# Kernel optimization log

Hardware: AMD Instinct MI355X
Metric: run time of the kernel (lower is better)

Reference implementation:

```python
import jax, jax.numpy as jnp
import numpy as np

N = 100000
E = 800000
D_IN = 128
D_OUT = 128
EPS = 1e-5


def setup_inputs() -> dict:
    key = jax.random.key(0)
    k = jax.random.split(key, 7)
    x = jax.random.normal(k[0], (N, D_IN), dtype=jnp.float32)
    edge_index = jax.random.randint(k[1], (2, E), 0, N, dtype=jnp.int64)
    # kaiming_uniform(a=sqrt(5)) on [out,in] -> bound = 1/sqrt(in_dim)
    bound = 1.0 / np.sqrt(D_IN)
    W_self = jax.random.uniform(k[2], (D_OUT, D_IN), minval=-bound, maxval=bound, dtype=jnp.float32)
    W_neigh = jax.random.uniform(k[3], (D_OUT, D_IN), minval=-bound, maxval=bound, dtype=jnp.float32)
    bias = jnp.zeros((D_OUT,), dtype=jnp.float32)
    gamma = jnp.ones((D_OUT,), dtype=jnp.float32)
    beta = jnp.zeros((D_OUT,), dtype=jnp.float32)
    return {"x": x, "edge_index": edge_index, "W_self": W_self,
            "W_neigh": W_neigh, "bias": bias, "gamma": gamma, "beta": beta}


def reference(x, edge_index, W_self, W_neigh, bias, gamma, beta):
    src, dst = edge_index[0], edge_index[1]
    # mean neighbor aggregation: segment-sum of gathered features / clamped degree
    agg = jax.ops.segment_sum(x[src], dst, num_segments=N)          # [N, D_IN]
    deg = jax.ops.segment_sum(jnp.ones_like(dst, dtype=x.dtype), dst, num_segments=N)
    neigh_mean = agg / jnp.maximum(deg, 1.0)[:, None]
    # dual linear + bias + ReLU
    out = jnp.einsum('nd,od->no', x, W_self) + jnp.einsum('nd,od->no', neigh_mean, W_neigh) + bias
    h = jax.nn.relu(out)
    # LayerNorm over last dim
    mu = jnp.mean(h, axis=-1, keepdims=True)
    var = jnp.var(h, axis=-1, keepdims=True)
    return (h - mu) * jax.lax.rsqrt(var + EPS) * gamma + beta
```

## Files before the change

kernel.cpp:

```cpp
#include <hip/hip_runtime.h>
#include <hip/hip_bf16.h>

#define N_NODES 100000
#define E_EDGES 800000
#define LN_EPS 1e-5f
#define WPAD 264

#define P_BLOCKS 256
#define EPB 3125
#define SLICE 64
#define NBK 1563
#define NBK_PAD 1792
#define OFFS_STRIDE 1564
#define QCAP 768
#define CONV_PER_BLOCK 12500

typedef __attribute__((ext_vector_type(4))) float f32x4;
typedef __attribute__((ext_vector_type(8))) short short8;

__device__ __forceinline__ unsigned short f2bf(float f) {
    __hip_bfloat16 h = __float2bfloat16(f);
    return *reinterpret_cast<unsigned short*>(&h);
}
__device__ __forceinline__ float bflo(unsigned int u) { return __uint_as_float(u << 16); }
__device__ __forceinline__ float bfhi(unsigned int u) { return __uint_as_float(u & 0xffff0000u); }

__global__ __launch_bounds__(256) void fill_part1(
    const float* __restrict__ x, const int* __restrict__ ei,
    unsigned short* __restrict__ xb, unsigned int* __restrict__ gstore,
    unsigned short* __restrict__ offs)
{
    const int t = threadIdx.x, b = blockIdx.x;
    if (b >= P_BLOCKS) {
        const float4* x4 = reinterpret_cast<const float4*>(x);
        ushort4* xb4 = reinterpret_cast<ushort4*>(xb);
        const int j0 = (b - P_BLOCKS) * CONV_PER_BLOCK;
        for (int j = t; j < CONV_PER_BLOCK; j += 256) {
            float4 v = x4[j0 + j];
            ushort4 o;
            o.x = f2bf(v.x); o.y = f2bf(v.y); o.z = f2bf(v.z); o.w = f2bf(v.w);
            xb4[j0 + j] = o;
        }
        return;
    }
    __shared__ unsigned long long eds[EPB];
    __shared__ unsigned int sorted_l[EPB];
    __shared__ int hist[NBK_PAD];
    __shared__ int starts[NBK_PAD + 1];
    __shared__ int partial[256];
    for (int i = t; i < NBK_PAD; i += 256) hist[i] = 0;
    __syncthreads();
    const int e0 = b * EPB;
    for (int i = t; i < EPB; i += 256) {
        unsigned src = (unsigned)ei[e0 + i];
        unsigned dst = (unsigned)ei[E_EDGES + e0 + i];
        unsigned bk = dst >> 6;
        eds[i] = ((unsigned long long)bk << 32) | (src << 6) | (dst & 63u);
        atomicAdd(&hist[bk], 1);
    }
    __syncthreads();
    int h[7], s = 0;
#pragma unroll
    for (int k = 0; k < 7; ++k) { h[k] = hist[t * 7 + k]; s += h[k]; }
    partial[t] = s;
    __syncthreads();
    for (int off = 1; off < 256; off <<= 1) {
        int v = (t >= off) ? partial[t - off] : 0;
        __syncthreads();
        partial[t] += v;
        __syncthreads();
    }
    int run = partial[t] - s;
#pragma unroll
    for (int k = 0; k < 7; ++k) { starts[t * 7 + k] = run; run += h[k]; }
    if (t == 255) starts[NBK_PAD] = run;
    __syncthreads();
    for (int i = t; i < NBK_PAD; i += 256) hist[i] = 0;
    __syncthreads();
    for (int i = t; i < EPB; i += 256) {
        unsigned long long u = eds[i];
        unsigned bk = (unsigned)(u >> 32);
        int p = starts[bk] + atomicAdd(&hist[bk], 1);
        sorted_l[p] = (unsigned int)u;
    }
    __syncthreads();
    for (int i = t; i < EPB; i += 256)
        gstore[b * EPB + i] = sorted_l[i];
    for (int i = t; i < OFFS_STRIDE; i += 256)
        offs[b * OFFS_STRIDE + i] = (unsigned short)starts[i];
}

__global__ __launch_bounds__(256) void agg2(
    const unsigned int* __restrict__ gstore, const unsigned short* __restrict__ offs,
    const unsigned short* __restrict__ xb, unsigned short* __restrict__ nb)
{
    __shared__ unsigned int sortedq[QCAP];
    __shared__ int cnt_l[SLICE];
    __shared__ int run_l[SLICE];
    __shared__ int qs_l[SLICE + 1];
    const int t = threadIdx.x, b = blockIdx.x;
    if (t < SLICE) { cnt_l[t] = 0; run_l[t] = 0; }
    __syncthreads();
    const int s0 = offs[t * OFFS_STRIDE + b];
    const int s1 = offs[t * OFFS_STRIDE + b + 1];
    const unsigned int* myrun = gstore + t * EPB;
    for (int j = s0; j < s1; ++j)
        atomicAdd(&cnt_l[myrun[j] & 63u], 1);
    __syncthreads();
    if (t < SLICE) {
        int inc = cnt_l[t];
        for (int off = 1; off < 64; off <<= 1) {
            int u = __shfl_up(inc, off);
            if (t >= off) inc += u;
        }
        qs_l[t + 1] = inc;
        if (t == 0) qs_l[0] = 0;
    }
    __syncthreads();
    for (int j = s0; j < s1; ++j) {
        unsigned rec = myrun[j];
        int p = qs_l[rec & 63u] + atomicAdd(&run_l[rec & 63u], 1);
        if (p < QCAP) sortedq[p] = rec;
    }
    __syncthreads();
    const int wave = t >> 6, lane = t & 63;
    const int subi = lane >> 4, chunk = lane & 15;
    const uint4* x4 = reinterpret_cast<const uint4*>(xb);
    for (int ln = wave * 16; ln < wave * 16 + 16; ++ln) {
        const int qb = qs_l[ln], cc = qs_l[ln + 1] - qb;
        float acc[8];
#pragma unroll
        for (int k = 0; k < 8; ++k) acc[k] = 0.f;
        for (int i = 0; i < cc; i += 4) {
            int idx = i + subi;
            if (idx < cc) {
                unsigned rec = sortedq[qb + idx];
                uint4 v = x4[(rec >> 6) * 16 + chunk];
                acc[0] += bflo(v.x); acc[1] += bfhi(v.x);
                acc[2] += bflo(v.y); acc[3] += bfhi(v.y);
                acc[4] += bflo(v.z); acc[5] += bfhi(v.z);
                acc[6] += bflo(v.w); acc[7] += bfhi(v.w);
            }
        }
#pragma unroll
        for (int k = 0; k < 8; ++k) {
            acc[k] += __shfl_xor(acc[k], 16);
            acc[k] += __shfl_xor(acc[k], 32);
        }
        const int node = b * SLICE + ln;
        if (subi == 0 && node < N_NODES) {
            float inv = 1.0f / (float)(cc > 1 ? cc : 1);
            uint4 o;
            o.x = ((unsigned)f2bf(acc[1] * inv) << 16) | f2bf(acc[0] * inv);
            o.y = ((unsigned)f2bf(acc[3] * inv) << 16) | f2bf(acc[2] * inv);
            o.z = ((unsigned)f2bf(acc[5] * inv) << 16) | f2bf(acc[4] * inv);
            o.w = ((unsigned)f2bf(acc[7] * inv) << 16) | f2bf(acc[6] * inv);
            reinterpret_cast<uint4*>(nb)[node * 16 + chunk] = o;
        }
    }
}

__global__ __launch_bounds__(256, 2) void fused_mfma(
    const unsigned short* __restrict__ xb, const unsigned short* __restrict__ nb,
    const float* __restrict__ Wself, const float* __restrict__ Wneigh,
    const float* __restrict__ bias, const float* __restrict__ gamma,
    const float* __restrict__ beta, float* __restrict__ out)
{
    __shared__ unsigned short WT[128][WPAD];
    const int t = threadIdx.x;
    const float4* Ws4 = reinterpret_cast<const float4*>(Wself);
    const float4* Wn4 = reinterpret_cast<const float4*>(Wneigh);
    for (int idx = t; idx < 4096; idx += 256) {
        int n = idx >> 5, k4 = (idx & 31) << 2;
        float4 a = Ws4[idx];
        float4 b = Wn4[idx];
        ushort4 ua, ub;
        ua.x = f2bf(a.x); ua.y = f2bf(a.y); ua.z = f2bf(a.z); ua.w = f2bf(a.w);
        ub.x = f2bf(b.x); ub.y = f2bf(b.y); ub.z = f2bf(b.z); ub.w = f2bf(b.w);
        *reinterpret_cast<ushort4*>(&WT[n][k4]) = ua;
        *reinterpret_cast<ushort4*>(&WT[n][128 + k4]) = ub;
    }
    __syncthreads();

    const int lane = t & 63, wave = t >> 6;
    const int l16 = lane & 15, quad = lane >> 4;
    float bia[8], gam[8], bet[8];
#pragma unroll
    for (int n = 0; n < 8; ++n) {
        int col = n * 16 + l16;
        bia[n] = bias[col]; gam[n] = gamma[col]; bet[n] = beta[col];
    }

    const int ntiles = (N_NODES + 255) / 256;
    for (int tile = blockIdx.x; tile < ntiles; tile += gridDim.x) {
        const int rowbase = tile * 256 + wave * 64;
        f32x4 acc[4][8];
#pragma unroll
        for (int m = 0; m < 4; ++m)
#pragma unroll
            for (int n = 0; n < 8; ++n) acc[m][n] = (f32x4)0.f;
        int rows[4];
#pragma unroll
        for (int m = 0; m < 4; ++m) {
            int r = rowbase + m * 16 + l16;
            rows[m] = r < N_NODES ? r : N_NODES - 1;
        }
#pragma unroll
        for (int kstep = 0; kstep < 8; ++kstep) {
            const unsigned short* Asrc = (kstep < 4) ? xb : nb;
            const int koff = (kstep & 3) * 32 + quad * 8;
            short8 a[4];
#pragma unroll
            for (int m = 0; m < 4; ++m)
                a[m] = *reinterpret_cast<const short8*>(Asrc + rows[m] * 128 + koff);
#pragma unroll
            for (int n = 0; n < 8; ++n) {
                short8 b = *reinterpret_cast<const short8*>(&WT[n * 16 + l16][kstep * 32 + quad * 8]);
#pragma unroll
                for (int m = 0; m < 4; ++m)
                    acc[m][n] = __builtin_amdgcn_mfma_f32_16x16x32_bf16(a[m], b, acc[m][n], 0, 0, 0);
            }
        }
#pragma unroll
        for (int m = 0; m < 4; ++m) {
#pragma unroll
            for (int r = 0; r < 4; ++r) {
                float h[8], s = 0.f, q = 0.f;
#pragma unroll
                for (int n = 0; n < 8; ++n) {
                    float v = acc[m][n][r] + bia[n];
                    v = fmaxf(v, 0.f);
                    h[n] = v; s += v; q += v * v;
                }
#pragma unroll
                for (int msk = 1; msk <= 8; msk <<= 1) {
                    s += __shfl_xor(s, msk);
                    q += __shfl_xor(q, msk);
                }
                const float mu = s * (1.f / 128.f);
                const float var = q * (1.f / 128.f) - mu * mu;
                const float rs = rsqrtf(var + LN_EPS);
                const int R = rowbase + m * 16 + quad * 4 + r;
                if (R < N_NODES) {
#pragma unroll
                    for (int n = 0; n < 8; ++n)
                        out[R * 128 + n * 16 + l16] = (h[n] - mu) * rs * gam[n] + bet[n];
                }
            }
        }
    }
}

extern "C" void kernel_launch(void* const* d_in, const int* in_sizes, int n_in,
                              void* d_out, int out_size, void* d_ws, size_t ws_size,
                              hipStream_t stream) {
    const float* x      = (const float*)d_in[0];
    const int*   ei     = (const int*)d_in[1];
    const float* Wself  = (const float*)d_in[2];
    const float* Wneigh = (const float*)d_in[3];
    const float* bias   = (const float*)d_in[4];
    const float* gamma  = (const float*)d_in[5];
    const float* beta   = (const float*)d_in[6];
    float* out = (float*)d_out;

    char* ws = (char*)d_ws;
    unsigned short* xb = (unsigned short*)ws;
    unsigned short* nb = (unsigned short*)(ws + 25600000);
    unsigned int* gstore = (unsigned int*)(ws + 51200000);
    unsigned short* offs = (unsigned short*)(ws + 54400000);

    fill_part1<<<512, 256, 0, stream>>>(x, ei, xb, gstore, offs);
    agg2<<<NBK, 256, 0, stream>>>(gstore, offs, xb, nb);
    const int ntiles = (N_NODES + 255) / 256;
    fused_mfma<<<ntiles, 256, 0, stream>>>(xb, nb, Wself, Wneigh, bias, gamma, beta, out);
}
```

Measured before the change: 204.5 us.

## Fuse neighbor aggregation with MFMA GEMM and LayerNorm in one kernel

```diff
diff --git a/kernel.cpp b/kernel.cpp
--- a/kernel.cpp
+++ b/kernel.cpp
@@ -4,7 +4,6 @@
 #define N_NODES 100000
 #define E_EDGES 800000
 #define LN_EPS 1e-5f
-#define WPAD 264
 
 #define P_BLOCKS 256
 #define EPB 3125
@@ -14,6 +13,8 @@
 #define OFFS_STRIDE 1564
 #define QCAP 768
 #define CONV_PER_BLOCK 12500
+#define TILE_BLKS 782
+#define NBPAD 136
 
 typedef __attribute__((ext_vector_type(4))) float f32x4;
 typedef __attribute__((ext_vector_type(8))) short short8;
@@ -27,8 +28,9 @@
 
 __global__ __launch_bounds__(256) void fill_part1(
     const float* __restrict__ x, const int* __restrict__ ei,
+    const float* __restrict__ Wself, const float* __restrict__ Wneigh,
     unsigned short* __restrict__ xb, unsigned int* __restrict__ gstore,
-    unsigned short* __restrict__ offs)
+    unsigned short* __restrict__ offs, unsigned short* __restrict__ Wswz)
 {
     const int t = threadIdx.x, b = blockIdx.x;
     if (b >= P_BLOCKS) {
@@ -41,6 +43,23 @@
             o.x = f2bf(v.x); o.y = f2bf(v.y); o.z = f2bf(v.z); o.w = f2bf(v.w);
             xb4[j0 + j] = o;
         }
+        if (b == P_BLOCKS) {
+            for (int idx = t; idx < 4096; idx += 256) {
+                int kstep = idx >> 9, n = (idx >> 6) & 7, lane = idx & 63;
+                int l16 = lane & 15, quad = lane >> 4;
+                int c = n * 16 + l16;
+                int kk = kstep * 32 + quad * 8;
+                const float* sp = (kk < 128) ? (Wself + c * 128 + kk)
+                                             : (Wneigh + c * 128 + kk - 128);
+                float4 v0 = *reinterpret_cast<const float4*>(sp);
+                float4 v1 = *reinterpret_cast<const float4*>(sp + 4);
+                ushort4 o0, o1;
+                o0.x = f2bf(v0.x); o0.y = f2bf(v0.y); o0.z = f2bf(v0.z); o0.w = f2bf(v0.w);
+                o1.x = f2bf(v1.x); o1.y = f2bf(v1.y); o1.z = f2bf(v1.z); o1.w = f2bf(v1.w);
+                *reinterpret_cast<ushort4*>(Wswz + idx * 8) = o0;
+                *reinterpret_cast<ushort4*>(Wswz + idx * 8 + 4) = o1;
+            }
+        }
         return;
     }
     __shared__ unsigned long long eds[EPB];
@@ -90,51 +109,60 @@
         offs[b * OFFS_STRIDE + i] = (unsigned short)starts[i];
 }
 
-__global__ __launch_bounds__(256) void agg2(
+__global__ __launch_bounds__(512, 6) void agg_gemm(
     const unsigned int* __restrict__ gstore, const unsigned short* __restrict__ offs,
-    const unsigned short* __restrict__ xb, unsigned short* __restrict__ nb)
+    const unsigned short* __restrict__ xb, const unsigned short* __restrict__ Wswz,
+    const float* __restrict__ bias, const float* __restrict__ gamma,
+    const float* __restrict__ beta, float* __restrict__ out)
 {
-    __shared__ unsigned int sortedq[QCAP];
-    __shared__ int cnt_l[SLICE];
-    __shared__ int run_l[SLICE];
-    __shared__ int qs_l[SLICE + 1];
+    __shared__ unsigned short nbT[128][NBPAD];
+    __shared__ unsigned int sortedq[2][QCAP];
+    __shared__ int cnt_l[2][SLICE];
+    __shared__ int run_l[2][SLICE];
+    __shared__ int qs_l[2][SLICE + 1];
     const int t = threadIdx.x, b = blockIdx.x;
-    if (t < SLICE) { cnt_l[t] = 0; run_l[t] = 0; }
-    __syncthreads();
-    const int s0 = offs[t * OFFS_STRIDE + b];
-    const int s1 = offs[t * OFFS_STRIDE + b + 1];
-    const unsigned int* myrun = gstore + t * EPB;
+    const int g = t >> 8, st = t & 255;
+    const int bucket = b * 2 + g;
+    if (st < SLICE) { cnt_l[g][st] = 0; run_l[g][st] = 0; }
+    __syncthreads();
+    int s0 = 0, s1 = 0;
+    if (bucket < NBK) {
+        s0 = offs[st * OFFS_STRIDE + bucket];
+        s1 = offs[st * OFFS_STRIDE + bucket + 1];
+    }
+    const unsigned int* myrun = gstore + st * EPB;
     for (int j = s0; j < s1; ++j)
-        atomicAdd(&cnt_l[myrun[j] & 63u], 1);
-    __syncthreads();
-    if (t < SLICE) {
-        int inc = cnt_l[t];
+        atomicAdd(&cnt_l[g][myrun[j] & 63u], 1);
+    __syncthreads();
+    if (st < SLICE) {
+        int inc = cnt_l[g][st];
         for (int off = 1; off < 64; off <<= 1) {
             int u = __shfl_up(inc, off);
-            if (t >= off) inc += u;
-        }
-        qs_l[t + 1] = inc;
-        if (t == 0) qs_l[0] = 0;
+            if (st >= off) inc += u;
+        }
+        qs_l[g][st + 1] = inc;
+        if (st == 0) qs_l[g][0] = 0;
     }
     __syncthreads();
     for (int j = s0; j < s1; ++j) {
         unsigned rec = myrun[j];
-        int p = qs_l[rec & 63u] + atomicAdd(&run_l[rec & 63u], 1);
-        if (p < QCAP) sortedq[p] = rec;
+        int p = qs_l[g][rec & 63u] + atomicAdd(&run_l[g][rec & 63u], 1);
+        if (p < QCAP) sortedq[g][p] = rec;
     }
     __syncthreads();
     const int wave = t >> 6, lane = t & 63;
     const int subi = lane >> 4, chunk = lane & 15;
+    const int gg = wave >> 2;
     const uint4* x4 = reinterpret_cast<const uint4*>(xb);
-    for (int ln = wave * 16; ln < wave * 16 + 16; ++ln) {
-        const int qb = qs_l[ln], cc = qs_l[ln + 1] - qb;
+    for (int ln = (wave & 3) * 16; ln < (wave & 3) * 16 + 16; ++ln) {
+        const int qb = qs_l[gg][ln], cc = qs_l[gg][ln + 1] - qb;
         float acc[8];
 #pragma unroll
         for (int k = 0; k < 8; ++k) acc[k] = 0.f;
         for (int i = 0; i < cc; i += 4) {
             int idx = i + subi;
             if (idx < cc) {
-                unsigned rec = sortedq[qb + idx];
+                unsigned rec = sortedq[gg][qb + idx];
                 uint4 v = x4[(rec >> 6) * 16 + chunk];
                 acc[0] += bflo(v.x); acc[1] += bfhi(v.x);
                 acc[2] += bflo(v.y); acc[3] += bfhi(v.y);
@@ -147,106 +175,65 @@
             acc[k] += __shfl_xor(acc[k], 16);
             acc[k] += __shfl_xor(acc[k], 32);
         }
-        const int node = b * SLICE + ln;
-        if (subi == 0 && node < N_NODES) {
+        if (subi == 0) {
             float inv = 1.0f / (float)(cc > 1 ? cc : 1);
             uint4 o;
             o.x = ((unsigned)f2bf(acc[1] * inv) << 16) | f2bf(acc[0] * inv);
             o.y = ((unsigned)f2bf(acc[3] * inv) << 16) | f2bf(acc[2] * inv);
             o.z = ((unsigned)f2bf(acc[5] * inv) << 16) | f2bf(acc[4] * inv);
             o.w = ((unsigned)f2bf(acc[7] * inv) << 16) | f2bf(acc[6] * inv);
-            reinterpret_cast<uint4*>(nb)[node * 16 + chunk] = o;
-        }
-    }
-}
-
-__global__ __launch_bounds__(256, 2) void fused_mfma(
-    const unsigned short* __restrict__ xb, const unsigned short* __restrict__ nb,
-    const float* __restrict__ Wself, const float* __restrict__ Wneigh,
-    const float* __restrict__ bias, const float* __restrict__ gamma,
-    const float* __restrict__ beta, float* __restrict__ out)
-{
-    __shared__ unsigned short WT[128][WPAD];
-    const int t = threadIdx.x;
-    const float4* Ws4 = reinterpret_cast<const float4*>(Wself);
-    const float4* Wn4 = reinterpret_cast<const float4*>(Wneigh);
-    for (int idx = t; idx < 4096; idx += 256) {
-        int n = idx >> 5, k4 = (idx & 31) << 2;
-        float4 a = Ws4[idx];
-        float4 b = Wn4[idx];
-        ushort4 ua, ub;
-        ua.x = f2bf(a.x); ua.y = f2bf(a.y); ua.z = f2bf(a.z); ua.w = f2bf(a.w);
-        ub.x = f2bf(b.x); ub.y = f2bf(b.y); ub.z = f2bf(b.z); ub.w = f2bf(b.w);
-        *reinterpret_cast<ushort4*>(&WT[n][k4]) = ua;
-        *reinterpret_cast<ushort4*>(&WT[n][128 + k4]) = ub;
-    }
-    __syncthreads();
-
-    const int lane = t & 63, wave = t >> 6;
+            *reinterpret_cast<uint4*>(&nbT[gg * 64 + ln][chunk * 8]) = o;
+        }
+    }
+    __syncthreads();
     const int l16 = lane & 15, quad = lane >> 4;
+    f32x4 acc[8];
+#pragma unroll
+    for (int n = 0; n < 8; ++n) acc[n] = (f32x4)0.f;
+    const int row = b * 128 + wave * 16 + l16;
+    const int rowc = row < N_NODES ? row : N_NODES - 1;
+    const short8* wsz = reinterpret_cast<const short8*>(Wswz);
+#pragma unroll
+    for (int kstep = 0; kstep < 8; ++kstep) {
+        short8 a;
+        if (kstep < 4)
+            a = *reinterpret_cast<const short8*>(xb + rowc * 128 + kstep * 32 + quad * 8);
+        else
+            a = *reinterpret_cast<const short8*>(&nbT[wave * 16 + l16][(kstep - 4) * 32 + quad * 8]);
+#pragma unroll
+        for (int n = 0; n < 8; ++n) {
+            short8 bb = wsz[(kstep * 8 + n) * 64 + lane];
+            acc[n] = __builtin_amdgcn_mfma_f32_16x16x32_bf16(a, bb, acc[n], 0, 0, 0);
+        }
+    }
     float bia[8], gam[8], bet[8];
 #pragma unroll
     for (int n = 0; n < 8; ++n) {
         int col = n * 16 + l16;
         bia[n] = bias[col]; gam[n] = gamma[col]; bet[n] = beta[col];
     }
-
-    const int ntiles = (N_NODES + 255) / 256;
-    for (int tile = blockIdx.x; tile < ntiles; tile += gridDim.x) {
-        const int rowbase = tile * 256 + wave * 64;
-        f32x4 acc[4][8];
-#pragma unroll
-        for (int m = 0; m < 4; ++m)
-#pragma unroll
-            for (int n = 0; n < 8; ++n) acc[m][n] = (f32x4)0.f;
-        int rows[4];
-#pragma unroll
-        for (int m = 0; m < 4; ++m) {
-            int r = rowbase + m * 16 + l16;
-            rows[m] = r < N_NODES ? r : N_NODES - 1;
-        }
-#pragma unroll
-        for (int kstep = 0; kstep < 8; ++kstep) {
-            const unsigned short* Asrc = (kstep < 4) ? xb : nb;
-            const int koff = (kstep & 3) * 32 + quad * 8;
-            short8 a[4];
-#pragma unroll
-            for (int m = 0; m < 4; ++m)
-                a[m] = *reinterpret_cast<const short8*>(Asrc + rows[m] * 128 + koff);
-#pragma unroll
-            for (int n = 0; n < 8; ++n) {
-                short8 b = *reinterpret_cast<const short8*>(&WT[n * 16 + l16][kstep * 32 + quad * 8]);
-#pragma unroll
-                for (int m = 0; m < 4; ++m)
-                    acc[m][n] = __builtin_amdgcn_mfma_f32_16x16x32_bf16(a[m], b, acc[m][n], 0, 0, 0);
-            }
-        }
-#pragma unroll
-        for (int m = 0; m < 4; ++m) {
-#pragma unroll
-            for (int r = 0; r < 4; ++r) {
-                float h[8], s = 0.f, q = 0.f;
-#pragma unroll
-                for (int n = 0; n < 8; ++n) {
-                    float v = acc[m][n][r] + bia[n];
-                    v = fmaxf(v, 0.f);
-                    h[n] = v; s += v; q += v * v;
-                }
-#pragma unroll
-                for (int msk = 1; msk <= 8; msk <<= 1) {
-                    s += __shfl_xor(s, msk);
-                    q += __shfl_xor(q, msk);
-                }
-                const float mu = s * (1.f / 128.f);
-                const float var = q * (1.f / 128.f) - mu * mu;
-                const float rs = rsqrtf(var + LN_EPS);
-                const int R = rowbase + m * 16 + quad * 4 + r;
-                if (R < N_NODES) {
-#pragma unroll
-                    for (int n = 0; n < 8; ++n)
-                        out[R * 128 + n * 16 + l16] = (h[n] - mu) * rs * gam[n] + bet[n];
-                }
-            }
+#pragma unroll
+    for (int r = 0; r < 4; ++r) {
+        float h[8], s = 0.f, q = 0.f;
+#pragma unroll
+        for (int n = 0; n < 8; ++n) {
+            float v = acc[n][r] + bia[n];
+            v = fmaxf(v, 0.f);
+            h[n] = v; s += v; q += v * v;
+        }
+#pragma unroll
+        for (int msk = 1; msk <= 8; msk <<= 1) {
+            s += __shfl_xor(s, msk);
+            q += __shfl_xor(q, msk);
+        }
+        const float mu = s * (1.f / 128.f);
+        const float var = q * (1.f / 128.f) - mu * mu;
+        const float rs = rsqrtf(var + LN_EPS);
+        const int R = b * 128 + wave * 16 + quad * 4 + r;
+        if (R < N_NODES) {
+#pragma unroll
+            for (int n = 0; n < 8; ++n)
+                out[R * 128 + n * 16 + l16] = (h[n] - mu) * rs * gam[n] + bet[n];
         }
     }
 }
@@ -265,12 +252,10 @@
 
     char* ws = (char*)d_ws;
     unsigned short* xb = (unsigned short*)ws;
-    unsigned short* nb = (unsigned short*)(ws + 25600000);
-    unsigned int* gstore = (unsigned int*)(ws + 51200000);
-    unsigned short* offs = (unsigned short*)(ws + 54400000);
-
-    fill_part1<<<512, 256, 0, stream>>>(x, ei, xb, gstore, offs);
-    agg2<<<NBK, 256, 0, stream>>>(gstore, offs, xb, nb);
-    const int ntiles = (N_NODES + 255) / 256;
-    fused_mfma<<<ntiles, 256, 0, stream>>>(xb, nb, Wself, Wneigh, bias, gamma, beta, out);
-}
+    unsigned int* gstore = (unsigned int*)(ws + 25600000);
+    unsigned short* offs = (unsigned short*)(ws + 28800000);
+    unsigned short* Wswz = (unsigned short*)(ws + 29601792);
+
+    fill_part1<<<512, 256, 0, stream>>>(x, ei, Wself, Wneigh, xb, gstore, offs, Wswz);
+    agg_gemm<<<TILE_BLKS, 512, 0, stream>>>(gstore, offs, xb, Wswz, bias, gamma, beta, out);
+}
```

Result: slower. 229.7 us (+12.3%).
